# Performance work log

Measured on AMD Instinct MI355X. Metric: run time of the kernel, lower is better.

Reference implementation:

```python
import jax, jax.numpy as jnp
import numpy as np

NUM_GROUPS = 8
EPS = 1e-5


def setup_inputs() -> dict:
    key = jax.random.key(0)
    ks = jax.random.split(key, 7)
    b, c, h, w = 4, 256, 64, 64
    x = jax.random.normal(ks[0], (b, c, h, w), dtype=jnp.float32)
    gamma = jnp.ones((c,), dtype=jnp.float32)
    beta = jnp.zeros((c,), dtype=jnp.float32)
    # 1x1 convs stored as [out_ch, in_ch] matrices
    w_qkv = jax.random.normal(ks[1], (3 * c, c), dtype=jnp.float32) * (1.0 / np.sqrt(c))
    b_qkv = jax.random.normal(ks[2], (3 * c,), dtype=jnp.float32) * 0.01
    # NOTE: original zero-inits proj; use small random weights so the op is non-trivial
    w_proj = jax.random.normal(ks[3], (c, c), dtype=jnp.float32) * (1.0 / np.sqrt(c))
    b_proj = jax.random.normal(ks[4], (c,), dtype=jnp.float32) * 0.01
    return {"x": x, "gamma": gamma, "beta": beta, "w_qkv": w_qkv,
            "b_qkv": b_qkv, "w_proj": w_proj, "b_proj": b_proj}


def _group_norm(x, gamma, beta):
    b, c, h, w = x.shape
    xg = x.reshape(b, NUM_GROUPS, c // NUM_GROUPS, h, w)
    mean = jnp.mean(xg, axis=(2, 3, 4), keepdims=True)
    var = jnp.var(xg, axis=(2, 3, 4), keepdims=True)
    xg = (xg - mean) * jax.lax.rsqrt(var + EPS)
    x = xg.reshape(b, c, h, w)
    return x * gamma[None, :, None, None] + beta[None, :, None, None]


def reference(x, gamma, beta, w_qkv, b_qkv, w_proj, b_proj):
    b, c, h, w = x.shape
    n = h * w
    residual = x
    xn = _group_norm(x, gamma, beta)
    # 1x1 conv qkv: [b, 3c, h, w]
    qkv = jnp.einsum('bchw,oc->bohw', xn, w_qkv) + b_qkv[None, :, None, None]
    q, k, v = jnp.split(qkv, 3, axis=1)
    q = q.reshape(b, c, n).transpose(0, 2, 1)   # [b, n, c]
    k = k.reshape(b, c, n)                       # [b, c, n]
    v = v.reshape(b, c, n).transpose(0, 2, 1)   # [b, n, c]
    scale = 1.0 / jnp.sqrt(jnp.asarray(c, dtype=x.dtype))
    attn = jnp.einsum('bic,bcj->bij', q, k) * scale    # [b, n, n]
    attn = jax.nn.softmax(attn, axis=-1)
    out = jnp.einsum('bij,bjc->bic', attn, v)          # [b, n, c]
    out = out.transpose(0, 2, 1).reshape(b, c, h, w)
    out = jnp.einsum('bchw,oc->bohw', out, w_proj) + b_proj[None, :, None, None]
    return out + residual
```

## Files before the change

### kernel.cpp

```cpp
#include <hip/hip_runtime.h>
#include <math.h>

#define BB   4
#define CC   256
#define NN   4096
#define GG   8
#define CPG  32
#define EPSV 1e-5f
#define SCALE 0.0625f
#define NSPLIT 4
#define PSTR 40

typedef __attribute__((ext_vector_type(8))) short bf16x8;
typedef __attribute__((ext_vector_type(4))) float f32x4;

struct alignas(8) us4 { unsigned short x, y, z, w; };

static __device__ __forceinline__ unsigned short f2bf(float f) {
    union { float f; unsigned int u; } a; a.f = f;
    unsigned int r = a.u + 0x7fffu + ((a.u >> 16) & 1u);
    return (unsigned short)(r >> 16);
}
static __device__ __forceinline__ void async16(const unsigned short* g, unsigned short* l) {
    __builtin_amdgcn_global_load_lds(
        (const __attribute__((address_space(1))) unsigned int*)g,
        (__attribute__((address_space(3))) unsigned int*)l,
        16, 0, 0);
}

__global__ __launch_bounds__(256) void prep_kernel(
    const float* __restrict__ x, const float* __restrict__ w_qkv,
    const float* __restrict__ w_proj, float* __restrict__ partials,
    unsigned short* __restrict__ wbf)
{
    const int tid = threadIdx.x;
    if (blockIdx.x >= 256) {
        int idx = ((blockIdx.x - 256)*256 + tid) * 4;
        float4 v;
        if (idx < 196608) v = *(const float4*)(w_qkv + idx);
        else              v = *(const float4*)(w_proj + (idx - 196608));
        us4 h = { f2bf(v.x), f2bf(v.y), f2bf(v.z), f2bf(v.w) };
        *(us4*)(wbf + idx) = h;
        return;
    }
    const int bg = blockIdx.x >> 3, slice = blockIdx.x & 7;
    const float4* base = (const float4*)(x + (size_t)bg*CPG*NN + slice*16384);
    float s = 0.f, sq = 0.f;
    for (int i = tid; i < 4096; i += 256) {
        float4 v = base[i];
        s  += v.x + v.y + v.z + v.w;
        sq += v.x*v.x + v.y*v.y + v.z*v.z + v.w*v.w;
    }
    __shared__ float ls[256], lq[256];
    ls[tid] = s; lq[tid] = sq;
    __syncthreads();
    for (int off = 128; off > 0; off >>= 1) {
        if (tid < off) { ls[tid] += ls[tid+off]; lq[tid] += lq[tid+off]; }
        __syncthreads();
    }
    if (tid == 0) { partials[blockIdx.x*2] = ls[0]; partials[blockIdx.x*2+1] = lq[0]; }
}

__global__ __launch_bounds__(256) void norm_t_kernel(
    const float* __restrict__ x, const float* __restrict__ gamma,
    const float* __restrict__ beta, const float* __restrict__ partials,
    unsigned short* __restrict__ xnT)
{
    const int n0 = blockIdx.x * 64;
    const int c0 = blockIdx.y * 64;
    const int b  = blockIdx.z;
    const int tid = threadIdx.x;
    __shared__ unsigned short T[64*68];
    __shared__ float ssc[64], ssh[64];
    if (tid < 64) {
        int c = c0 + tid;
        int bg = b*GG + (c >> 5);
        float s = 0.f, sq = 0.f;
        for (int i = 0; i < 8; i++) {
            s  += partials[(bg*8 + i)*2];
            sq += partials[(bg*8 + i)*2 + 1];
        }
        const float cnt = (float)(CPG*NN);
        float mean = s / cnt;
        float var  = sq / cnt - mean*mean;
        float rstd = rsqrtf(var + EPSV);
        float g = gamma[c], be = beta[c];
        ssc[tid] = rstd*g;
        ssh[tid] = be - mean*rstd*g;
    }
    __syncthreads();
    {
        int cl = tid >> 4, n4 = tid & 15;
        for (int i = 0; i < 4; i++) {
            int c = cl + i*16;
            float4 v = *(const float4*)(x + ((size_t)(b*CC + c0 + c))*NN + n0 + n4*4);
            float sc = ssc[c], sh = ssh[c];
            T[(n4*4+0)*68 + c] = f2bf(v.x*sc + sh);
            T[(n4*4+1)*68 + c] = f2bf(v.y*sc + sh);
            T[(n4*4+2)*68 + c] = f2bf(v.z*sc + sh);
            T[(n4*4+3)*68 + c] = f2bf(v.w*sc + sh);
        }
    }
    __syncthreads();
    {
        int nl = tid >> 3, cs = tid & 7;
        for (int i = 0; i < 2; i++) {
            int n = nl + i*32;
            *(bf16x8*)(xnT + ((size_t)(b*NN + n0 + n))*CC + c0 + cs*8) =
                *(const bf16x8*)&T[n*68 + cs*8];
        }
    }
}

__global__ __launch_bounds__(256) void qkv_mfma_kernel(
    const unsigned short* __restrict__ xnT, const unsigned short* __restrict__ wbf,
    const float* __restrict__ b_qkv,
    unsigned short* __restrict__ qsw, unsigned short* __restrict__ ksw,
    unsigned short* __restrict__ vsw)
{
    const int tid  = threadIdx.x;
    const int wave = tid >> 6, lane = tid & 63;
    const int lrow = lane & 15, quad = lane >> 4;
    const int R0   = blockIdx.x * 128;
    const int b    = blockIdx.x >> 5;
    const int nb0  = (blockIdx.x & 31) * 128;
    const int oBase = blockIdx.y * 64;
    const int which = oBase >> 8;
    const int o0l   = oBase & 255;
    const bool isV  = (which == 2);
    const int wn = wave >> 1, wo = wave & 1;

    const unsigned short* Abase;
    const unsigned short* Bbase;
    if (!isV) {
        Abase = wbf + ((size_t)(oBase + lrow))*CC + quad*8;
        Bbase = xnT + ((size_t)(R0 + wave*32 + lrow))*CC + quad*8;
    } else {
        Abase = xnT + ((size_t)(R0 + wn*64 + lrow))*CC + quad*8;
        Bbase = wbf + ((size_t)(oBase + wo*32 + lrow))*CC + quad*8;
    }

    f32x4 acc[4][2];
    for (int s = 0; s < 4; s++) for (int t = 0; t < 2; t++)
        acc[s][t] = (f32x4){0.f, 0.f, 0.f, 0.f};

    for (int c0 = 0; c0 < CC; c0 += 32) {
        bf16x8 af[4], bfr[2];
        for (int s = 0; s < 4; s++) af[s]  = *(const bf16x8*)(Abase + s*16*CC + c0);
        for (int t = 0; t < 2; t++) bfr[t] = *(const bf16x8*)(Bbase + t*16*CC + c0);
        for (int s = 0; s < 4; s++)
            for (int t = 0; t < 2; t++)
                acc[s][t] = __builtin_amdgcn_mfma_f32_16x16x32_bf16(af[s], bfr[t], acc[s][t], 0, 0, 0);
    }

    __shared__ unsigned short lds[8192];

    if (!isV) {
        const float sc = (which == 0) ? SCALE : 1.0f;
        for (int s = 0; s < 4; s++) {
            float bias[4];
            for (int r = 0; r < 4; r++) bias[r] = b_qkv[oBase + s*16 + quad*4 + r];
            for (int t = 0; t < 2; t++) {
                us4 h;
                h.x = f2bf((acc[s][t][0] + bias[0]) * sc);
                h.y = f2bf((acc[s][t][1] + bias[1]) * sc);
                h.z = f2bf((acc[s][t][2] + bias[2]) * sc);
                h.w = f2bf((acc[s][t][3] + bias[3]) * sc);
                int chunk = (wave*2 + t)*2 + (s>>1);
                int pos = (((s*2 + (quad>>1)) & 3)*16 + lrow)*8 + (quad&1)*4;
                *(us4*)&lds[chunk*512 + pos] = h;
            }
        }
    } else {
        for (int s = 0; s < 4; s++)
            for (int t = 0; t < 2; t++) {
                int oc = o0l + wo*32 + t*16 + lrow;
                float bias = b_qkv[512 + oc];
                us4 h;
                h.x = f2bf(acc[s][t][0] + bias);
                h.y = f2bf(acc[s][t][1] + bias);
                h.z = f2bf(acc[s][t][2] + bias);
                h.w = f2bf(acc[s][t][3] + bias);
                int chunk = (wn*2 + (s>>1))*4 + wo*2 + t;
                int pos = (((s&1)*2 + (quad>>1))*16 + lrow)*8 + (quad&1)*4;
                *(us4*)&lds[chunk*512 + pos] = h;
            }
    }
    __syncthreads();

    if (!isV) {
        unsigned short* dst = (which == 0) ? qsw : ksw;
        for (int it = 0; it < 4; it++) {
            int f = it*4 + (tid>>6);
            int ng_l = f >> 1, kk_l = f & 1;
            size_t off = ((size_t)(b*256 + (nb0>>4) + ng_l)*8 + (o0l>>5) + kk_l)*512 + lane*8;
            *(bf16x8*)(dst + off) = *(const bf16x8*)&lds[f*512 + lane*8];
        }
    } else {
        for (int it = 0; it < 4; it++) {
            int f = it*4 + (tid>>6);
            int jg_l = f >> 2, ns_l = f & 3;
            size_t off = ((size_t)(b*128 + (nb0>>5) + jg_l)*16 + (o0l>>4) + ns_l)*512 + lane*8;
            *(bf16x8*)(vsw + off) = *(const bf16x8*)&lds[f*512 + lane*8];
        }
    }
}

__global__ __launch_bounds__(256, 2) void attn_mfma_kernel(
    const unsigned short* __restrict__ qsw, const unsigned short* __restrict__ ksw,
    const unsigned short* __restrict__ vsw,
    unsigned short* __restrict__ opart, float* __restrict__ lpart)
{
    const int tid  = threadIdx.x;
    const int wave = tid >> 6, lane = tid & 63;
    const int lrow = lane & 15, quad = lane >> 4;
    const int bx    = blockIdx.x;
    const int split = bx & 3;
    const int ig    = (bx >> 2) & 31;
    const int b     = bx >> 7;
    const int i0w   = ig*128 + wave*32;
    const int koff  = split * (NN / NSPLIT);
    const int NT    = (NN / NSPLIT) / 32;

    __shared__ unsigned short ldsK[2][8192];
    __shared__ unsigned short ldsV[2][8192];
    __shared__ unsigned short ldsP[4][32*PSTR];

    bf16x8 qf[2][8];
    {
        const unsigned short* qb = qsw + ((size_t)b << 20) + (size_t)i0w*256 + lane*8;
        for (int g = 0; g < 2; g++)
            for (int kk = 0; kk < 8; kk++)
                qf[g][kk] = *(const bf16x8*)(qb + g*4096 + kk*512);
    }

    f32x4 o_acc[2][16];
    for (int g = 0; g < 2; g++)
        for (int ns = 0; ns < 16; ns++)
            o_acc[g][ns] = (f32x4){0.f, 0.f, 0.f, 0.f};
    float lsum[2] = {0.f, 0.f};

    const unsigned short* kp = ksw + ((size_t)b << 20) + (size_t)koff*256 + wave*2048 + lane*8;
    const unsigned short* vp = vsw + ((size_t)b << 20) + (size_t)koff*256 + wave*2048 + lane*8;

    for (int t = 0; t < 4; t++) {
        async16(kp + t*512, ldsK[0] + wave*2048 + t*512);
        async16(vp + t*512, ldsV[0] + wave*2048 + t*512);
    }
    asm volatile("s_waitcnt vmcnt(0)" ::: "memory");
    __builtin_amdgcn_s_barrier();

    for (int jt = 0; jt < NT; jt++) {
        const int cur = jt & 1, nxt = cur ^ 1;

        if (jt + 1 < NT) {
            for (int t = 0; t < 4; t++) {
                async16(kp + (size_t)(jt+1)*8192 + t*512, ldsK[nxt] + wave*2048 + t*512);
                async16(vp + (size_t)(jt+1)*8192 + t*512, ldsV[nxt] + wave*2048 + t*512);
            }
        }

        f32x4 s[2][2];
        for (int jg = 0; jg < 2; jg++)
            for (int g = 0; g < 2; g++)
                s[jg][g] = (f32x4){0.f, 0.f, 0.f, 0.f};
        const unsigned short* lk = ldsK[cur];
        __builtin_amdgcn_s_setprio(1);
        for (int jg = 0; jg < 2; jg++)
            for (int kk = 0; kk < 8; kk++) {
                bf16x8 kf = *(const bf16x8*)(lk + (jg*8 + kk)*512 + lane*8);
                s[jg][0] = __builtin_amdgcn_mfma_f32_16x16x32_bf16(kf, qf[0][kk], s[jg][0], 0, 0, 0);
                s[jg][1] = __builtin_amdgcn_mfma_f32_16x16x32_bf16(kf, qf[1][kk], s[jg][1], 0, 0, 0);
            }
        __builtin_amdgcn_s_setprio(0);

        unsigned short* pw = ldsP[wave];
        for (int jg = 0; jg < 2; jg++)
            for (int g = 0; g < 2; g++) {
                float p0 = __expf(s[jg][g][0]);
                float p1 = __expf(s[jg][g][1]);
                float p2 = __expf(s[jg][g][2]);
                float p3 = __expf(s[jg][g][3]);
                lsum[g] += p0 + p1 + p2 + p3;
                us4 h = { f2bf(p0), f2bf(p1), f2bf(p2), f2bf(p3) };
                *(us4*)(pw + (g*16 + lrow)*PSTR + jg*16 + quad*4) = h;
            }

        bf16x8 pa[2];
        for (int g = 0; g < 2; g++)
            pa[g] = *(const bf16x8*)(pw + (g*16 + lrow)*PSTR + quad*8);

        const unsigned short* lv = ldsV[cur];
        __builtin_amdgcn_s_setprio(1);
        for (int ns = 0; ns < 16; ns++) {
            bf16x8 vf = *(const bf16x8*)(lv + ns*512 + lane*8);
            o_acc[0][ns] = __builtin_amdgcn_mfma_f32_16x16x32_bf16(pa[0], vf, o_acc[0][ns], 0, 0, 0);
            o_acc[1][ns] = __builtin_amdgcn_mfma_f32_16x16x32_bf16(pa[1], vf, o_acc[1][ns], 0, 0, 0);
        }
        __builtin_amdgcn_s_setprio(0);

        asm volatile("s_waitcnt vmcnt(0) lgkmcnt(0)" ::: "memory");
        __builtin_amdgcn_s_barrier();
    }

    for (int g = 0; g < 2; g++) {
        float v = lsum[g];
        v += __shfl_xor(v, 16);
        v += __shfl_xor(v, 32);
        lsum[g] = v;
    }

    unsigned short* reg = &ldsV[0][0] + wave*4096;
    const size_t planeb = ((size_t)(split*BB + b)) << 20;
    for (int g = 0; g < 2; g++) {
        for (int ns = 0; ns < 16; ns++) {
            int kk = ns >> 1;
            int posbase = ((ns & 1)*2 + (lrow >> 3))*128 + (lrow & 7) + quad*32;
            for (int r = 0; r < 4; r++)
                reg[kk*512 + posbase + r*8] = f2bf(o_acc[g][ns][r]);
        }
        unsigned short* dst = opart + planeb + ((size_t)((i0w >> 4) + g))*4096;
        for (int kk = 0; kk < 8; kk++)
            *(bf16x8*)(dst + kk*512 + lane*8) = *(const bf16x8*)(reg + kk*512 + lane*8);
    }
    if (quad == 0)
        for (int g = 0; g < 2; g++)
            lpart[(size_t)(split*BB + b)*NN + i0w + g*16 + lrow] = lsum[g];
}

__global__ __launch_bounds__(256, 2) void proj_mfma_kernel(
    const unsigned short* __restrict__ opart, const float* __restrict__ lpart,
    const unsigned short* __restrict__ w2bf, const float* __restrict__ b_proj,
    const float* __restrict__ x, float* __restrict__ out)
{
    const int tid  = threadIdx.x;
    const int wave = tid >> 6, lane = tid & 63;
    const int lrow = lane & 15, quad = lane >> 4;
    const int rt = blockIdx.x >> 1;
    const int oh = blockIdx.x & 1;
    const int b  = rt >> 6;
    const int n0 = (rt & 63) * 64;

    const int rg = (n0 >> 4) + wave;
    const unsigned short* Ab = opart + ((size_t)b << 20) + (size_t)rg*4096 + lane*8;
    const size_t pstride = (size_t)BB << 20;

    f32x4 acc[8];
    for (int t = 0; t < 8; t++) acc[t] = (f32x4){0.f, 0.f, 0.f, 0.f};

    for (int kk = 0; kk < 8; kk++) {
        bf16x8 bfr[8];
        for (int t = 0; t < 8; t++)
            bfr[t] = *(const bf16x8*)(w2bf +
                ((size_t)(oh*128 + t*16 + lrow))*CC + kk*32 + quad*8);
        for (int sp = 0; sp < NSPLIT; sp++) {
            bf16x8 af = *(const bf16x8*)(Ab + (size_t)sp*pstride + kk*512);
            for (int t = 0; t < 8; t++)
                acc[t] = __builtin_amdgcn_mfma_f32_16x16x32_bf16(af, bfr[t], acc[t], 0, 0, 0);
        }
    }

    float sinv[4];
    for (int r = 0; r < 4; r++) {
        int n = n0 + wave*16 + quad*4 + r;
        float l = 0.f;
        for (int sp = 0; sp < NSPLIT; sp++)
            l += lpart[(size_t)(sp*BB + b)*NN + n];
        sinv[r] = 1.0f / l;
    }

    for (int t = 0; t < 8; t++) {
        int o = oh*128 + t*16 + lrow;
        int n = n0 + wave*16 + quad*4;
        size_t idx = ((size_t)(b*CC + o))*NN + n;
        float bias = b_proj[o];
        float4 xv = *(const float4*)(x + idx);
        float4 ov;
        ov.x = acc[t][0]*sinv[0] + bias + xv.x;
        ov.y = acc[t][1]*sinv[1] + bias + xv.y;
        ov.z = acc[t][2]*sinv[2] + bias + xv.z;
        ov.w = acc[t][3]*sinv[3] + bias + xv.w;
        *(float4*)(out + idx) = ov;
    }
}

extern "C" void kernel_launch(void* const* d_in, const int* in_sizes, int n_in,
                              void* d_out, int out_size, void* d_ws, size_t ws_size,
                              hipStream_t stream) {
    const float* x      = (const float*)d_in[0];
    const float* gamma  = (const float*)d_in[1];
    const float* beta   = (const float*)d_in[2];
    const float* w_qkv  = (const float*)d_in[3];
    const float* b_qkv  = (const float*)d_in[4];
    const float* w_proj = (const float*)d_in[5];
    const float* b_proj = (const float*)d_in[6];
    float* out = (float*)d_out;

    const size_t plane = (size_t)BB * NN * CC;
    unsigned short* xnT = (unsigned short*)d_ws;
    unsigned short* qsw = xnT + plane;
    unsigned short* ksw = qsw + plane;
    unsigned short* vsw = ksw + plane;
    unsigned short* wbf = vsw + plane;
    unsigned short* opart = wbf + 262144;
    float* lpart    = (float*)(opart + (size_t)NSPLIT*plane);
    float* partials = lpart + (size_t)NSPLIT*BB*NN;

    prep_kernel<<<512, 256, 0, stream>>>(x, w_qkv, w_proj, partials, wbf);

    dim3 gnt(64, 4, BB);
    norm_t_kernel<<<gnt, 256, 0, stream>>>(x, gamma, beta, partials, xnT);

    dim3 gq(128, 12);
    qkv_mfma_kernel<<<gq, 256, 0, stream>>>(xnT, wbf, b_qkv, qsw, ksw, vsw);

    attn_mfma_kernel<<<BB*32*NSPLIT, 256, 0, stream>>>(qsw, ksw, vsw, opart, lpart);

    proj_mfma_kernel<<<512, 256, 0, stream>>>(opart, lpart, wbf + 196608, b_proj, x, out);
}
```

Measured before the change: 220.5 us.

## Software-pipeline attention: overlap QK of next tile with PV of previous

Restructures the attention main loop so that each iteration computes the score MFMAs for the current K tile while running the P·V MFMAs for the previous tile. The exponentials and bf16 packing of the new scores are interleaved into the PV MFMA loop. K stays single-buffered and V moves to a triple buffer with rotating pointers, so total LDS stays about the same. The goal is to hide softmax VALU work and load latency behind matrix instructions. The cost is more complex wait-count logic: on the last iteration vmcnt(4) may not cover the final V tile load, which is a possible race.

```diff
diff --git a/kernel.cpp b/kernel.cpp
--- a/kernel.cpp
+++ b/kernel.cpp
@@ -222,8 +222,8 @@
     const int koff  = split * (NN / NSPLIT);
     const int NT    = (NN / NSPLIT) / 32;
 
-    __shared__ unsigned short ldsK[2][8192];
-    __shared__ unsigned short ldsV[2][8192];
+    __shared__ unsigned short ldsK[8192];
+    __shared__ unsigned short ldsVbuf[3][8192];
     __shared__ unsigned short ldsP[4][32*PSTR];
 
     bf16x8 qf[2][8];
@@ -243,38 +243,40 @@
     const unsigned short* kp = ksw + ((size_t)b << 20) + (size_t)koff*256 + wave*2048 + lane*8;
     const unsigned short* vp = vsw + ((size_t)b << 20) + (size_t)koff*256 + wave*2048 + lane*8;
 
+    unsigned short* Vprev = ldsVbuf[0];
+    unsigned short* Vcur  = ldsVbuf[1];
+    unsigned short* Vnext = ldsVbuf[2];
+
+    unsigned short* pw = ldsP[wave];
+
     for (int t = 0; t < 4; t++) {
-        async16(kp + t*512, ldsK[0] + wave*2048 + t*512);
-        async16(vp + t*512, ldsV[0] + wave*2048 + t*512);
+        async16(kp + t*512, ldsK + wave*2048 + t*512);
+        async16(vp + t*512, ldsVbuf[0] + wave*2048 + t*512);
     }
     asm volatile("s_waitcnt vmcnt(0)" ::: "memory");
     __builtin_amdgcn_s_barrier();
 
-    for (int jt = 0; jt < NT; jt++) {
-        const int cur = jt & 1, nxt = cur ^ 1;
-
-        if (jt + 1 < NT) {
-            for (int t = 0; t < 4; t++) {
-                async16(kp + (size_t)(jt+1)*8192 + t*512, ldsK[nxt] + wave*2048 + t*512);
-                async16(vp + (size_t)(jt+1)*8192 + t*512, ldsV[nxt] + wave*2048 + t*512);
-            }
-        }
-
+    {
         f32x4 s[2][2];
         for (int jg = 0; jg < 2; jg++)
             for (int g = 0; g < 2; g++)
                 s[jg][g] = (f32x4){0.f, 0.f, 0.f, 0.f};
-        const unsigned short* lk = ldsK[cur];
         __builtin_amdgcn_s_setprio(1);
         for (int jg = 0; jg < 2; jg++)
             for (int kk = 0; kk < 8; kk++) {
-                bf16x8 kf = *(const bf16x8*)(lk + (jg*8 + kk)*512 + lane*8);
+                bf16x8 kf = *(const bf16x8*)(ldsK + (jg*8 + kk)*512 + lane*8);
                 s[jg][0] = __builtin_amdgcn_mfma_f32_16x16x32_bf16(kf, qf[0][kk], s[jg][0], 0, 0, 0);
                 s[jg][1] = __builtin_amdgcn_mfma_f32_16x16x32_bf16(kf, qf[1][kk], s[jg][1], 0, 0, 0);
             }
         __builtin_amdgcn_s_setprio(0);
-
-        unsigned short* pw = ldsP[wave];
+        asm volatile("s_waitcnt lgkmcnt(0)" ::: "memory");
+        __builtin_amdgcn_s_barrier();
+
+        for (int t = 0; t < 4; t++)
+            async16(kp + 8192 + t*512, ldsK + wave*2048 + t*512);
+        for (int t = 0; t < 4; t++)
+            async16(vp + 8192 + t*512, ldsVbuf[1] + wave*2048 + t*512);
+
         for (int jg = 0; jg < 2; jg++)
             for (int g = 0; g < 2; g++) {
                 float p0 = __expf(s[jg][g][0]);
@@ -285,22 +287,74 @@
                 us4 h = { f2bf(p0), f2bf(p1), f2bf(p2), f2bf(p3) };
                 *(us4*)(pw + (g*16 + lrow)*PSTR + jg*16 + quad*4) = h;
             }
+        asm volatile("s_waitcnt vmcnt(4)" ::: "memory");
+        __builtin_amdgcn_s_barrier();
+    }
+
+    for (int jt = 1; jt < NT; jt++) {
+        f32x4 s[2][2];
+        for (int jg = 0; jg < 2; jg++)
+            for (int g = 0; g < 2; g++)
+                s[jg][g] = (f32x4){0.f, 0.f, 0.f, 0.f};
+        __builtin_amdgcn_s_setprio(1);
+        for (int jg = 0; jg < 2; jg++)
+            for (int kk = 0; kk < 8; kk++) {
+                bf16x8 kf = *(const bf16x8*)(ldsK + (jg*8 + kk)*512 + lane*8);
+                s[jg][0] = __builtin_amdgcn_mfma_f32_16x16x32_bf16(kf, qf[0][kk], s[jg][0], 0, 0, 0);
+                s[jg][1] = __builtin_amdgcn_mfma_f32_16x16x32_bf16(kf, qf[1][kk], s[jg][1], 0, 0, 0);
+            }
+        __builtin_amdgcn_s_setprio(0);
+        asm volatile("s_waitcnt lgkmcnt(0)" ::: "memory");
+        __builtin_amdgcn_s_barrier();
+
+        if (jt + 1 < NT) {
+            for (int t = 0; t < 4; t++)
+                async16(kp + (size_t)(jt+1)*8192 + t*512, ldsK + wave*2048 + t*512);
+            for (int t = 0; t < 4; t++)
+                async16(vp + (size_t)(jt+1)*8192 + t*512, Vnext + wave*2048 + t*512);
+        }
 
         bf16x8 pa[2];
         for (int g = 0; g < 2; g++)
             pa[g] = *(const bf16x8*)(pw + (g*16 + lrow)*PSTR + quad*8);
 
-        const unsigned short* lv = ldsV[cur];
+        __builtin_amdgcn_s_setprio(1);
+        #pragma unroll
+        for (int ns = 0; ns < 16; ns++) {
+            bf16x8 vf = *(const bf16x8*)(Vprev + ns*512 + lane*8);
+            o_acc[0][ns] = __builtin_amdgcn_mfma_f32_16x16x32_bf16(pa[0], vf, o_acc[0][ns], 0, 0, 0);
+            o_acc[1][ns] = __builtin_amdgcn_mfma_f32_16x16x32_bf16(pa[1], vf, o_acc[1][ns], 0, 0, 0);
+            if (ns < 4) {
+                const int jg = ns >> 1, g = ns & 1;
+                float p0 = __expf(s[jg][g][0]);
+                float p1 = __expf(s[jg][g][1]);
+                float p2 = __expf(s[jg][g][2]);
+                float p3 = __expf(s[jg][g][3]);
+                lsum[g] += p0 + p1 + p2 + p3;
+                us4 h = { f2bf(p0), f2bf(p1), f2bf(p2), f2bf(p3) };
+                *(us4*)(pw + (g*16 + lrow)*PSTR + jg*16 + quad*4) = h;
+            }
+        }
+        __builtin_amdgcn_s_setprio(0);
+
+        asm volatile("s_waitcnt vmcnt(4)" ::: "memory");
+        __builtin_amdgcn_s_barrier();
+
+        unsigned short* tmp = Vprev;
+        Vprev = Vcur; Vcur = Vnext; Vnext = tmp;
+    }
+
+    {
+        bf16x8 pa[2];
+        for (int g = 0; g < 2; g++)
+            pa[g] = *(const bf16x8*)(pw + (g*16 + lrow)*PSTR + quad*8);
         __builtin_amdgcn_s_setprio(1);
         for (int ns = 0; ns < 16; ns++) {
-            bf16x8 vf = *(const bf16x8*)(lv + ns*512 + lane*8);
+            bf16x8 vf = *(const bf16x8*)(Vprev + ns*512 + lane*8);
             o_acc[0][ns] = __builtin_amdgcn_mfma_f32_16x16x32_bf16(pa[0], vf, o_acc[0][ns], 0, 0, 0);
             o_acc[1][ns] = __builtin_amdgcn_mfma_f32_16x16x32_bf16(pa[1], vf, o_acc[1][ns], 0, 0, 0);
         }
         __builtin_amdgcn_s_setprio(0);
-
-        asm volatile("s_waitcnt vmcnt(0) lgkmcnt(0)" ::: "memory");
-        __builtin_amdgcn_s_barrier();
     }
 
     for (int g = 0; g < 2; g++) {
@@ -310,7 +364,9 @@
         lsum[g] = v;
     }
 
-    unsigned short* reg = &ldsV[0][0] + wave*4096;
+    __syncthreads();
+
+    unsigned short* reg = &ldsVbuf[0][0] + wave*4096;
     const size_t planeb = ((size_t)(split*BB + b)) << 20;
     for (int g = 0; g < 2; g++) {
         for (int ns = 0; ns < 16; ns++) {
```

Result: slower. 232.3 us (+5.3%).

## Single-buffer attention K/V tiles, raise occupancy, and split keys eightfold when workspace allows

Applied to the files above, without the earlier changes.

The attention kernel drops double-buffered K/V LDS tiles and uses one shared buffer, loading each tile synchronously before compute. This halves LDS use and lets launch bounds request three blocks per CU. When the workspace is large enough, the key dimension is split eight ways instead of four, giving more blocks but more partial outputs for the projection kernel to reduce. The cost is that load/compute overlap within a block is lost, and the projection kernel reads twice the partial data.

```diff
diff --git a/kernel.cpp b/kernel.cpp
--- a/kernel.cpp
+++ b/kernel.cpp
@@ -8,7 +8,6 @@
 #define CPG  32
 #define EPSV 1e-5f
 #define SCALE 0.0625f
-#define NSPLIT 4
 #define PSTR 40
 
 typedef __attribute__((ext_vector_type(8))) short bf16x8;
@@ -206,7 +205,8 @@
     }
 }
 
-__global__ __launch_bounds__(256, 2) void attn_mfma_kernel(
+template<int NS>
+__global__ __launch_bounds__(256, 3) void attn_mfma_kernel(
     const unsigned short* __restrict__ qsw, const unsigned short* __restrict__ ksw,
     const unsigned short* __restrict__ vsw,
     unsigned short* __restrict__ opart, float* __restrict__ lpart)
@@ -215,16 +215,17 @@
     const int wave = tid >> 6, lane = tid & 63;
     const int lrow = lane & 15, quad = lane >> 4;
     const int bx    = blockIdx.x;
-    const int split = bx & 3;
-    const int ig    = (bx >> 2) & 31;
-    const int b     = bx >> 7;
+    const int split = bx & (NS-1);
+    const int ig    = (bx / NS) & 31;
+    const int b     = bx / (NS*32);
     const int i0w   = ig*128 + wave*32;
-    const int koff  = split * (NN / NSPLIT);
-    const int NT    = (NN / NSPLIT) / 32;
-
-    __shared__ unsigned short ldsK[2][8192];
-    __shared__ unsigned short ldsV[2][8192];
+    const int koff  = split * (NN / NS);
+    const int NT    = (NN / NS) / 32;
+
+    __shared__ unsigned short ldsKV[2][8192];
     __shared__ unsigned short ldsP[4][32*PSTR];
+    unsigned short* ldsK = ldsKV[0];
+    unsigned short* ldsV = ldsKV[1];
 
     bf16x8 qf[2][8];
     {
@@ -243,38 +244,29 @@
     const unsigned short* kp = ksw + ((size_t)b << 20) + (size_t)koff*256 + wave*2048 + lane*8;
     const unsigned short* vp = vsw + ((size_t)b << 20) + (size_t)koff*256 + wave*2048 + lane*8;
 
-    for (int t = 0; t < 4; t++) {
-        async16(kp + t*512, ldsK[0] + wave*2048 + t*512);
-        async16(vp + t*512, ldsV[0] + wave*2048 + t*512);
-    }
-    asm volatile("s_waitcnt vmcnt(0)" ::: "memory");
-    __builtin_amdgcn_s_barrier();
+    unsigned short* pw = ldsP[wave];
 
     for (int jt = 0; jt < NT; jt++) {
-        const int cur = jt & 1, nxt = cur ^ 1;
-
-        if (jt + 1 < NT) {
-            for (int t = 0; t < 4; t++) {
-                async16(kp + (size_t)(jt+1)*8192 + t*512, ldsK[nxt] + wave*2048 + t*512);
-                async16(vp + (size_t)(jt+1)*8192 + t*512, ldsV[nxt] + wave*2048 + t*512);
-            }
-        }
+        for (int t = 0; t < 4; t++) {
+            async16(kp + (size_t)jt*8192 + t*512, ldsK + wave*2048 + t*512);
+            async16(vp + (size_t)jt*8192 + t*512, ldsV + wave*2048 + t*512);
+        }
+        asm volatile("s_waitcnt vmcnt(0)" ::: "memory");
+        __builtin_amdgcn_s_barrier();
 
         f32x4 s[2][2];
         for (int jg = 0; jg < 2; jg++)
             for (int g = 0; g < 2; g++)
                 s[jg][g] = (f32x4){0.f, 0.f, 0.f, 0.f};
-        const unsigned short* lk = ldsK[cur];
         __builtin_amdgcn_s_setprio(1);
         for (int jg = 0; jg < 2; jg++)
             for (int kk = 0; kk < 8; kk++) {
-                bf16x8 kf = *(const bf16x8*)(lk + (jg*8 + kk)*512 + lane*8);
+                bf16x8 kf = *(const bf16x8*)(ldsK + (jg*8 + kk)*512 + lane*8);
                 s[jg][0] = __builtin_amdgcn_mfma_f32_16x16x32_bf16(kf, qf[0][kk], s[jg][0], 0, 0, 0);
                 s[jg][1] = __builtin_amdgcn_mfma_f32_16x16x32_bf16(kf, qf[1][kk], s[jg][1], 0, 0, 0);
             }
         __builtin_amdgcn_s_setprio(0);
 
-        unsigned short* pw = ldsP[wave];
         for (int jg = 0; jg < 2; jg++)
             for (int g = 0; g < 2; g++) {
                 float p0 = __expf(s[jg][g][0]);
@@ -290,16 +282,15 @@
         for (int g = 0; g < 2; g++)
             pa[g] = *(const bf16x8*)(pw + (g*16 + lrow)*PSTR + quad*8);
 
-        const unsigned short* lv = ldsV[cur];
         __builtin_amdgcn_s_setprio(1);
         for (int ns = 0; ns < 16; ns++) {
-            bf16x8 vf = *(const bf16x8*)(lv + ns*512 + lane*8);
+            bf16x8 vf = *(const bf16x8*)(ldsV + ns*512 + lane*8);
             o_acc[0][ns] = __builtin_amdgcn_mfma_f32_16x16x32_bf16(pa[0], vf, o_acc[0][ns], 0, 0, 0);
             o_acc[1][ns] = __builtin_amdgcn_mfma_f32_16x16x32_bf16(pa[1], vf, o_acc[1][ns], 0, 0, 0);
         }
         __builtin_amdgcn_s_setprio(0);
 
-        asm volatile("s_waitcnt vmcnt(0) lgkmcnt(0)" ::: "memory");
+        asm volatile("s_waitcnt lgkmcnt(0)" ::: "memory");
         __builtin_amdgcn_s_barrier();
     }
 
@@ -310,7 +301,7 @@
         lsum[g] = v;
     }
 
-    unsigned short* reg = &ldsV[0][0] + wave*4096;
+    unsigned short* reg = &ldsKV[0][0] + wave*4096;
     const size_t planeb = ((size_t)(split*BB + b)) << 20;
     for (int g = 0; g < 2; g++) {
         for (int ns = 0; ns < 16; ns++) {
@@ -328,6 +319,7 @@
             lpart[(size_t)(split*BB + b)*NN + i0w + g*16 + lrow] = lsum[g];
 }
 
+template<int NS>
 __global__ __launch_bounds__(256, 2) void proj_mfma_kernel(
     const unsigned short* __restrict__ opart, const float* __restrict__ lpart,
     const unsigned short* __restrict__ w2bf, const float* __restrict__ b_proj,
@@ -353,7 +345,7 @@
         for (int t = 0; t < 8; t++)
             bfr[t] = *(const bf16x8*)(w2bf +
                 ((size_t)(oh*128 + t*16 + lrow))*CC + kk*32 + quad*8);
-        for (int sp = 0; sp < NSPLIT; sp++) {
+        for (int sp = 0; sp < NS; sp++) {
             bf16x8 af = *(const bf16x8*)(Ab + (size_t)sp*pstride + kk*512);
             for (int t = 0; t < 8; t++)
                 acc[t] = __builtin_amdgcn_mfma_f32_16x16x32_bf16(af, bfr[t], acc[t], 0, 0, 0);
@@ -364,7 +356,7 @@
     for (int r = 0; r < 4; r++) {
         int n = n0 + wave*16 + quad*4 + r;
         float l = 0.f;
-        for (int sp = 0; sp < NSPLIT; sp++)
+        for (int sp = 0; sp < NS; sp++)
             l += lpart[(size_t)(sp*BB + b)*NN + n];
         sinv[r] = 1.0f / l;
     }
@@ -397,14 +389,22 @@
     float* out = (float*)d_out;
 
     const size_t plane = (size_t)BB * NN * CC;
+
+    auto ws_need = [&](int ns) -> size_t {
+        size_t us = 4*plane + 262144 + (size_t)ns*plane;
+        size_t fl = (size_t)ns*BB*NN + 512;
+        return us*2 + fl*4;
+    };
+    const int NS = (ws_size >= ws_need(8)) ? 8 : 4;
+
     unsigned short* xnT = (unsigned short*)d_ws;
     unsigned short* qsw = xnT + plane;
     unsigned short* ksw = qsw + plane;
     unsigned short* vsw = ksw + plane;
     unsigned short* wbf = vsw + plane;
     unsigned short* opart = wbf + 262144;
-    float* lpart    = (float*)(opart + (size_t)NSPLIT*plane);
-    float* partials = lpart + (size_t)NSPLIT*BB*NN;
+    float* lpart    = (float*)(opart + (size_t)NS*plane);
+    float* partials = lpart + (size_t)NS*BB*NN;
 
     prep_kernel<<<512, 256, 0, stream>>>(x, w_qkv, w_proj, partials, wbf);
 
@@ -414,7 +414,11 @@
     dim3 gq(128, 12);
     qkv_mfma_kernel<<<gq, 256, 0, stream>>>(xnT, wbf, b_qkv, qsw, ksw, vsw);
 
-    attn_mfma_kernel<<<BB*32*NSPLIT, 256, 0, stream>>>(qsw, ksw, vsw, opart, lpart);
-
-    proj_mfma_kernel<<<512, 256, 0, stream>>>(opart, lpart, wbf + 196608, b_proj, x, out);
-}
+    if (NS == 8) {
+        attn_mfma_kernel<8><<<BB*32*8, 256, 0, stream>>>(qsw, ksw, vsw, opart, lpart);
+        proj_mfma_kernel<8><<<512, 256, 0, stream>>>(opart, lpart, wbf + 196608, b_proj, x, out);
+    } else {
+        attn_mfma_kernel<4><<<BB*32*4, 256, 0, stream>>>(qsw, ksw, vsw, opart, lpart);
+        proj_mfma_kernel<4><<<512, 256, 0, stream>>>(opart, lpart, wbf + 196608, b_proj, x, out);
+    }
+}
```

After: 705.0 us. +219.8%, slower.
